# Performance work log

Hardware: AMD Instinct MI355X
Metric: run time of the kernel (lower is better)

Reference implementation:

```python
import jax, jax.numpy as jnp
import numpy as np

B, F, E, H, D = 8192, 40, 128, 4, 4
DH = E // H  # per-head attention dim
STD = 0.05   # all params init N(0, 0.05) in the torch module (including LayerNorm!)


def setup_inputs() -> dict:
    key = jax.random.key(0)
    ks = jax.random.split(key, 7)
    inputs = jax.random.normal(ks[0], (B, F, E), dtype=jnp.float32)
    # domain ids in [1, D] so every row belongs to some domain (torch masks domain_ids == i+1)
    domain_ids = jax.random.randint(ks[1], (B,), 1, D + 1)
    W_Queries = jax.random.normal(ks[2], (D, E, E), dtype=jnp.float32) * STD  # domain_W_Queries
    W_Value = jax.random.normal(ks[3], (E, E), dtype=jnp.float32) * STD
    W_Res = jax.random.normal(ks[4], (E, E), dtype=jnp.float32) * STD
    ln_gamma = jax.random.normal(ks[5], (D, E), dtype=jnp.float32) * STD  # per-domain LayerNorm weight
    ln_beta = jax.random.normal(ks[6], (D, E), dtype=jnp.float32) * STD   # per-domain LayerNorm bias
    return dict(inputs=inputs, domain_ids=domain_ids, W_Queries=W_Queries,
                W_Value=W_Value, W_Res=W_Res, ln_gamma=ln_gamma, ln_beta=ln_beta)


def reference(inputs, domain_ids, W_Queries, W_Value, W_Res, ln_gamma, ln_beta):
    d = domain_ids - 1  # (B,) zero-based domain index
    # value projection is shared across domains
    v = jnp.einsum('bfe,eh->bfh', inputs, W_Value).reshape(B, F, H, DH)
    # merge='no': the key projection is domain_W_Queries[0] for EVERY domain (source quirk)
    k = jnp.einsum('bfe,eh->bfh', inputs, W_Queries[0]).reshape(B, F, H, DH)
    # per-sample domain-routed query projection
    Wq_b = W_Queries[d]  # (B, E, E) gather
    q = jnp.einsum('bfe,beh->bfh', inputs, Wq_b).reshape(B, F, H, DH)
    # scaled multi-head attention over the field axis (F x F per head)
    scores = jnp.einsum('bihd,bjhd->bhij', q, k) / np.float32(np.sqrt(DH))
    attn = jax.nn.softmax(scores, axis=-1)  # attn_dropout is identity in eval mode
    out = jnp.einsum('bhij,bjhd->bihd', attn, v).reshape(B, F, E)
    # residual projection + relu
    out = jax.nn.relu(out + jnp.einsum('bfe,eh->bfh', inputs, W_Res))
    # per-domain LayerNorm (eps=1e-6), params gathered per sample
    mean = out.mean(axis=-1, keepdims=True)
    var = ((out - mean) ** 2).mean(axis=-1, keepdims=True)
    normed = (out - mean) / jnp.sqrt(var + 1e-6)
    return normed * ln_gamma[d][:, None, :] + ln_beta[d][:, None, :]
```

## Files before the change

kernel.cpp:

```cpp
#include <hip/hip_runtime.h>
#include <hip/hip_bf16.h>

typedef __attribute__((ext_vector_type(4))) float f32x4;
typedef __attribute__((ext_vector_type(8))) short s16x8;
typedef unsigned long long u64;

namespace {
constexpr int B_   = 8192;
constexpr int NT   = 256;
constexpr int SPB  = 8;
constexpr int NBLK = B_ / SPB;
constexpr int XS_SH  = 48 * 136;
constexpr int RED_B  = XS_SH * 2;
constexpr int OUT_B  = RED_B + 48 * 4 * 2 * 4;
constexpr int OSTR   = 132;
constexpr int POOL_B = OUT_B + 40 * OSTR * 4;
}

__device__ __forceinline__ ushort f2b(float f) {
    union { __hip_bfloat16 h; ushort u; } cv;
    cv.h = __float2bfloat16(f);
    return cv.u;
}
__device__ __forceinline__ u64 pack4(f32x4 v) {
    return (u64)f2b(v[0]) | ((u64)f2b(v[1]) << 16)
         | ((u64)f2b(v[2]) << 32) | ((u64)f2b(v[3]) << 48);
}
#define MFMA(a, b, c) __builtin_amdgcn_mfma_f32_16x16x32_bf16((a), (b), (c), 0, 0, 0)

__device__ __forceinline__ s16x8 remap(u64 A, u64 B, int sl0, int sl1, bool hi) {
    const int a0 = (int)A, a1 = (int)(A >> 32);
    const int b0 = (int)B, b1 = (int)(B >> 32);
    const int pa0 = __shfl(a0, sl0), pa2 = __shfl(a0, sl1);
    const int pa1 = __shfl(a1, sl0), pa3 = __shfl(a1, sl1);
    const int pb0 = __shfl(b0, sl0), pb2 = __shfl(b0, sl1);
    const int pb1 = __shfl(b1, sl0), pb3 = __shfl(b1, sl1);
    union { int i[4]; s16x8 v; } r;
    r.i[0] = hi ? pb0 : pa0;
    r.i[1] = hi ? pb1 : pa1;
    r.i[2] = hi ? pb2 : pa2;
    r.i[3] = hi ? pb3 : pa3;
    return r.v;
}
__device__ __forceinline__ s16x8 remapA(u64 A, int sl0, int sl1, bool hi) {
    const int a0 = (int)A, a1 = (int)(A >> 32);
    const int pa0 = __shfl(a0, sl0), pa2 = __shfl(a0, sl1);
    const int pa1 = __shfl(a1, sl0), pa3 = __shfl(a1, sl1);
    union { int i[4]; s16x8 v; } r;
    r.i[0] = hi ? 0 : pa0;
    r.i[1] = hi ? 0 : pa1;
    r.i[2] = hi ? 0 : pa2;
    r.i[3] = hi ? 0 : pa3;
    return r.v;
}

__global__ void convert_w(const float* __restrict__ Wq,
                          const float* __restrict__ Wv,
                          const float* __restrict__ Wr,
                          ushort* __restrict__ Wt)
{
    int idx = blockIdx.x * 256 + threadIdx.x;
    if (idx >= 6 * 16384) return;
    int m = idx >> 14, r = idx & 16383, n = r >> 7, k = r & 127;
    float v;
    if (m < 4)       v = Wq[(size_t)m * 16384 + k * 128 + n];
    else if (m == 4) v = Wv[k * 128 + n];
    else             v = Wr[k * 128 + n];
    Wt[idx] = f2b(v);
}

__global__ __launch_bounds__(NT, 2)
void mdr_fused7(const float* __restrict__ inputs,
                const int* __restrict__ dom,
                const ushort* __restrict__ Wt,
                const float* __restrict__ ln_g,
                const float* __restrict__ ln_b,
                float* __restrict__ out)
{
    __shared__ __align__(16) char pool[POOL_B];
    ushort* sp = reinterpret_cast<ushort*>(pool);
    float* red = reinterpret_cast<float*>(pool + RED_B);
    float* ost = reinterpret_cast<float*>(pool + OUT_B);

    const int t = threadIdx.x;
    const int w = t >> 6, l = t & 63;
    const int lr = l & 15, lc = l >> 4;
    const int sl0 = lr + 32 * (lc & 1);
    const int sl1 = sl0 + 16;
    const bool hi = lc >= 2;
    const int h = w;
    const size_t s0 = (size_t)blockIdx.x * SPB;
    const float4* in4 = reinterpret_cast<const float4*>(inputs);
    float4* out4g = reinterpret_cast<float4*>(out);

    {
        const int row = 40 + (t >> 5), c = (t & 31) * 4;
        *reinterpret_cast<u64*>(&sp[row * 136 + c]) = 0ull;
    }

    float4 xp[5];
    #pragma unroll
    for (int j = 0; j < 5; ++j)
        xp[j] = in4[s0 * 1280 + t + 256 * j];

    #pragma unroll 1
    for (int s = 0; s < SPB; ++s) {
        #pragma unroll
        for (int j = 0; j < 5; ++j) {
            const int idx4 = t + 256 * j;
            const int row = idx4 >> 5, c4 = idx4 & 31;
            u64 pk = (u64)f2b(xp[j].x) | ((u64)f2b(xp[j].y) << 16)
                   | ((u64)f2b(xp[j].z) << 32) | ((u64)f2b(xp[j].w) << 48);
            *reinterpret_cast<u64*>(&sp[row * 136 + c4 * 4]) = pk;
        }
        const int d = dom[s0 + s] - 1;
        __syncthreads();

        const ushort* wq = Wt + (size_t)d * 16384 + (h * 32) * 128;
        const ushort* wk = Wt + (h * 32) * 128;
        const ushort* wv = Wt + (size_t)4 * 16384 + (h * 32) * 128;
        const ushort* wr = Wt + (size_t)5 * 16384 + (h * 32) * 128;
        const int wo = lr * 128 + lc * 8;

        f32x4 aq[2][3], ak[2][3];
        #pragma unroll
        for (int nt = 0; nt < 2; ++nt)
            #pragma unroll
            for (int rt = 0; rt < 3; ++rt) {
                aq[nt][rt] = f32x4{0.f, 0.f, 0.f, 0.f};
                ak[nt][rt] = f32x4{0.f, 0.f, 0.f, 0.f};
            }
        #pragma unroll
        for (int kk = 0; kk < 4; ++kk) {
            s16x8 xf[3];
            #pragma unroll
            for (int rt = 0; rt < 3; ++rt)
                xf[rt] = *reinterpret_cast<const s16x8*>(&sp[(rt * 16 + lr) * 136 + kk * 32 + lc * 8]);
            #pragma unroll
            for (int nt = 0; nt < 2; ++nt) {
                const int o = nt * 2048 + wo + kk * 32;
                const s16x8 qf = *reinterpret_cast<const s16x8*>(wq + o);
                const s16x8 kf = *reinterpret_cast<const s16x8*>(wk + o);
                #pragma unroll
                for (int rt = 0; rt < 3; ++rt) {
                    aq[nt][rt] = MFMA(qf, xf[rt], aq[nt][rt]);
                    ak[nt][rt] = MFMA(kf, xf[rt], ak[nt][rt]);
                }
            }
        }
        s16x8 qfr[3], kfr[3];
        #pragma unroll
        for (int tt = 0; tt < 3; ++tt) {
            qfr[tt] = remap(pack4(aq[0][tt]), pack4(aq[1][tt]), sl0, sl1, hi);
            kfr[tt] = remap(pack4(ak[0][tt]), pack4(ak[1][tt]), sl0, sl1, hi);
        }

        f32x4 av[3][2], ar[2][3];
        #pragma unroll
        for (int nt = 0; nt < 2; ++nt)
            #pragma unroll
            for (int rt = 0; rt < 3; ++rt) {
                av[rt][nt] = f32x4{0.f, 0.f, 0.f, 0.f};
                ar[nt][rt] = f32x4{0.f, 0.f, 0.f, 0.f};
            }
        #pragma unroll
        for (int kk = 0; kk < 4; ++kk) {
            s16x8 xf[3];
            #pragma unroll
            for (int rt = 0; rt < 3; ++rt)
                xf[rt] = *reinterpret_cast<const s16x8*>(&sp[(rt * 16 + lr) * 136 + kk * 32 + lc * 8]);
            #pragma unroll
            for (int nt = 0; nt < 2; ++nt) {
                const int o = nt * 2048 + wo + kk * 32;
                const s16x8 vf = *reinterpret_cast<const s16x8*>(wv + o);
                const s16x8 rf = *reinterpret_cast<const s16x8*>(wr + o);
                #pragma unroll
                for (int rt = 0; rt < 3; ++rt) {
                    av[rt][nt] = MFMA(xf[rt], vf, av[rt][nt]);
                    ar[nt][rt] = MFMA(rf, xf[rt], ar[nt][rt]);
                }
            }
        }
        u64 pkV[3][2];
        #pragma unroll
        for (int rt = 0; rt < 3; ++rt)
            #pragma unroll
            for (int nt = 0; nt < 2; ++nt)
                pkV[rt][nt] = pack4(av[rt][nt]);

        const float scale = 0.17677669529663689f;
        u64 pkP[3][3];
        float inv[3];
        #pragma unroll
        for (int it = 0; it < 3; ++it) {
            f32x4 sr[3];
            #pragma unroll
            for (int jt = 0; jt < 3; ++jt) {
                f32x4 z = {0.f, 0.f, 0.f, 0.f};
                sr[jt] = MFMA(kfr[jt], qfr[it], z);
            }
            float sum = 0.f;
            #pragma unroll
            for (int jt = 0; jt < 3; ++jt) {
                f32x4 pv;
                #pragma unroll
                for (int reg = 0; reg < 4; ++reg) {
                    float p = (jt == 2 && lc >= 2) ? 0.f : __expf(sr[jt][reg] * scale);
                    pv[reg] = p;
                    sum += p;
                }
                pkP[it][jt] = pack4(pv);
            }
            sum += __shfl_xor(sum, 16);
            sum += __shfl_xor(sum, 32);
            inv[it] = 1.f / sum;
        }

        if (s + 1 < SPB) {
            #pragma unroll
            for (int j = 0; j < 5; ++j)
                xp[j] = in4[(s0 + s + 1) * 1280 + t + 256 * j];
        }

        f32x4 o[2][3];
        #pragma unroll
        for (int et = 0; et < 2; ++et)
            #pragma unroll
            for (int it = 0; it < 3; ++it)
                o[et][it] = f32x4{0.f, 0.f, 0.f, 0.f};
        #pragma unroll
        for (int kk = 0; kk < 2; ++kk) {
            s16x8 vfr[2], pfr[3];
            #pragma unroll
            for (int et = 0; et < 2; ++et)
                vfr[et] = kk ? remapA(pkV[2][et], sl0, sl1, hi)
                             : remap(pkV[0][et], pkV[1][et], sl0, sl1, hi);
            #pragma unroll
            for (int it = 0; it < 3; ++it)
                pfr[it] = kk ? remapA(pkP[it][2], sl0, sl1, hi)
                             : remap(pkP[it][0], pkP[it][1], sl0, sl1, hi);
            #pragma unroll
            for (int et = 0; et < 2; ++et)
                #pragma unroll
                for (int it = 0; it < 3; ++it)
                    o[et][it] = MFMA(vfr[et], pfr[it], o[et][it]);
        }

        #pragma unroll
        for (int it = 0; it < 3; ++it) {
            const bool valid = !(it == 2 && lr >= 8);
            float sa = 0.f, qa2 = 0.f;
            float4 yv[2];
            #pragma unroll
            for (int et = 0; et < 2; ++et)
                #pragma unroll
                for (int reg = 0; reg < 4; ++reg) {
                    float yy = fmaxf(fmaf(o[et][it][reg], inv[it], ar[et][it][reg]), 0.f);
                    (&yv[et].x)[reg] = yy;
                    sa += yy;
                    qa2 = fmaf(yy, yy, qa2);
                }
            sa  += __shfl_xor(sa, 16);   sa  += __shfl_xor(sa, 32);
            qa2 += __shfl_xor(qa2, 16);  qa2 += __shfl_xor(qa2, 32);
            if (lc == 0)
                *reinterpret_cast<float2*>(&red[((it * 16 + lr) * 4 + w) * 2]) =
                    make_float2(sa, qa2);
            if (valid) {
                #pragma unroll
                for (int et = 0; et < 2; ++et)
                    *reinterpret_cast<float4*>(&ost[(it * 16 + lr) * OSTR + h * 32 + et * 16 + 4 * lc]) = yv[et];
            }
        }
        __syncthreads();

        const int c4r = t & 31;
        const float4 gvr = *reinterpret_cast<const float4*>(&ln_g[d * 128 + c4r * 4]);
        const float4 bvr = *reinterpret_cast<const float4*>(&ln_b[d * 128 + c4r * 4]);
        const size_t b4 = (s0 + s) * 1280;
        #pragma unroll
        for (int j5 = 0; j5 < 5; ++j5) {
            const int idx = j5 * 256 + t;
            const int row = idx >> 5;
            const float4 r01 = *reinterpret_cast<const float4*>(&red[row * 8]);
            const float4 r23 = *reinterpret_cast<const float4*>(&red[row * 8 + 4]);
            const float sa = r01.x + r01.z + r23.x + r23.z;
            const float q2 = r01.y + r01.w + r23.y + r23.w;
            const float mean = sa * (1.f / 128.f);
            const float rstd = rsqrtf(q2 * (1.f / 128.f) - mean * mean + 1e-6f);
            const float4 v = *reinterpret_cast<const float4*>(&ost[row * OSTR + c4r * 4]);
            float4 ov;
            ov.x = (v.x - mean) * rstd * gvr.x + bvr.x;
            ov.y = (v.y - mean) * rstd * gvr.y + bvr.y;
            ov.z = (v.z - mean) * rstd * gvr.z + bvr.z;
            ov.w = (v.w - mean) * rstd * gvr.w + bvr.w;
            out4g[b4 + idx] = ov;
        }
    }
}

extern "C" void kernel_launch(void* const* d_in, const int* in_sizes, int n_in,
                              void* d_out, int out_size, void* d_ws, size_t ws_size,
                              hipStream_t stream)
{
    const float* inputs = (const float*)d_in[0];
    const int*   dm     = (const int*)d_in[1];
    const float* Wq     = (const float*)d_in[2];
    const float* Wv     = (const float*)d_in[3];
    const float* Wr     = (const float*)d_in[4];
    const float* g      = (const float*)d_in[5];
    const float* bt     = (const float*)d_in[6];
    float* outp         = (float*)d_out;
    ushort* Wt          = (ushort*)d_ws;

    convert_w<<<(6 * 16384 + 255) / 256, 256, 0, stream>>>(Wq, Wv, Wr, Wt);
    mdr_fused7<<<NBLK, NT, 0, stream>>>(inputs, dm, Wt, g, bt, outp);
}
```

Before: 152.9 us.

## Fuse Q/K/V/R projection loops, halve samples per block, use raw v_exp

Merges the two projection k-loops into one pass so each x fragment read from LDS feeds all four weight MFMAs. Accumulators are zero-initialized via the first MFMA instead of explicit zeroing. Samples per block drop from 8 to 4, doubling the grid to 2048 blocks. The softmax exp is computed with an inline v_exp_f32 using a log2-prescaled constant. The fused loop keeps 24 accumulators live at once, which raises register pressure under the occupancy-2 launch bound and risks spills.

```diff
diff --git a/kernel.cpp b/kernel.cpp
--- a/kernel.cpp
+++ b/kernel.cpp
@@ -8,7 +8,7 @@
 namespace {
 constexpr int B_   = 8192;
 constexpr int NT   = 256;
-constexpr int SPB  = 8;
+constexpr int SPB  = 4;
 constexpr int NBLK = B_ / SPB;
 constexpr int XS_SH  = 48 * 136;
 constexpr int RED_B  = XS_SH * 2;
@@ -70,7 +70,7 @@
 }
 
 __global__ __launch_bounds__(NT, 2)
-void mdr_fused7(const float* __restrict__ inputs,
+void mdr_fused8(const float* __restrict__ inputs,
                 const int* __restrict__ dom,
                 const ushort* __restrict__ Wt,
                 const float* __restrict__ ln_g,
@@ -122,14 +122,8 @@
         const ushort* wr = Wt + (size_t)5 * 16384 + (h * 32) * 128;
         const int wo = lr * 128 + lc * 8;
 
-        f32x4 aq[2][3], ak[2][3];
-        #pragma unroll
-        for (int nt = 0; nt < 2; ++nt)
-            #pragma unroll
-            for (int rt = 0; rt < 3; ++rt) {
-                aq[nt][rt] = f32x4{0.f, 0.f, 0.f, 0.f};
-                ak[nt][rt] = f32x4{0.f, 0.f, 0.f, 0.f};
-            }
+        f32x4 aq[2][3], ak[2][3], av[3][2], ar[2][3];
+        const f32x4 zz = {0.f, 0.f, 0.f, 0.f};
         #pragma unroll
         for (int kk = 0; kk < 4; ++kk) {
             s16x8 xf[3];
@@ -141,10 +135,14 @@
                 const int o = nt * 2048 + wo + kk * 32;
                 const s16x8 qf = *reinterpret_cast<const s16x8*>(wq + o);
                 const s16x8 kf = *reinterpret_cast<const s16x8*>(wk + o);
+                const s16x8 vf = *reinterpret_cast<const s16x8*>(wv + o);
+                const s16x8 rf = *reinterpret_cast<const s16x8*>(wr + o);
                 #pragma unroll
                 for (int rt = 0; rt < 3; ++rt) {
-                    aq[nt][rt] = MFMA(qf, xf[rt], aq[nt][rt]);
-                    ak[nt][rt] = MFMA(kf, xf[rt], ak[nt][rt]);
+                    aq[nt][rt] = MFMA(qf, xf[rt], kk == 0 ? zz : aq[nt][rt]);
+                    ak[nt][rt] = MFMA(kf, xf[rt], kk == 0 ? zz : ak[nt][rt]);
+                    av[rt][nt] = MFMA(xf[rt], vf, kk == 0 ? zz : av[rt][nt]);
+                    ar[nt][rt] = MFMA(rf, xf[rt], kk == 0 ? zz : ar[nt][rt]);
                 }
             }
         }
@@ -154,33 +152,6 @@
             qfr[tt] = remap(pack4(aq[0][tt]), pack4(aq[1][tt]), sl0, sl1, hi);
             kfr[tt] = remap(pack4(ak[0][tt]), pack4(ak[1][tt]), sl0, sl1, hi);
         }
-
-        f32x4 av[3][2], ar[2][3];
-        #pragma unroll
-        for (int nt = 0; nt < 2; ++nt)
-            #pragma unroll
-            for (int rt = 0; rt < 3; ++rt) {
-                av[rt][nt] = f32x4{0.f, 0.f, 0.f, 0.f};
-                ar[nt][rt] = f32x4{0.f, 0.f, 0.f, 0.f};
-            }
-        #pragma unroll
-        for (int kk = 0; kk < 4; ++kk) {
-            s16x8 xf[3];
-            #pragma unroll
-            for (int rt = 0; rt < 3; ++rt)
-                xf[rt] = *reinterpret_cast<const s16x8*>(&sp[(rt * 16 + lr) * 136 + kk * 32 + lc * 8]);
-            #pragma unroll
-            for (int nt = 0; nt < 2; ++nt) {
-                const int o = nt * 2048 + wo + kk * 32;
-                const s16x8 vf = *reinterpret_cast<const s16x8*>(wv + o);
-                const s16x8 rf = *reinterpret_cast<const s16x8*>(wr + o);
-                #pragma unroll
-                for (int rt = 0; rt < 3; ++rt) {
-                    av[rt][nt] = MFMA(xf[rt], vf, av[rt][nt]);
-                    ar[nt][rt] = MFMA(rf, xf[rt], ar[nt][rt]);
-                }
-            }
-        }
         u64 pkV[3][2];
         #pragma unroll
         for (int rt = 0; rt < 3; ++rt)
@@ -188,7 +159,7 @@
             for (int nt = 0; nt < 2; ++nt)
                 pkV[rt][nt] = pack4(av[rt][nt]);
 
-        const float scale = 0.17677669529663689f;
+        const float l2scale = 0.2550348615f;
         u64 pkP[3][3];
         float inv[3];
         #pragma unroll
@@ -205,7 +176,13 @@
                 f32x4 pv;
                 #pragma unroll
                 for (int reg = 0; reg < 4; ++reg) {
-                    float p = (jt == 2 && lc >= 2) ? 0.f : __expf(sr[jt][reg] * scale);
+                    float p;
+                    if (jt == 2 && lc >= 2) {
+                        p = 0.f;
+                    } else {
+                        const float e2 = sr[jt][reg] * l2scale;
+                        asm("v_exp_f32 %0, %1" : "=v"(p) : "v"(e2));
+                    }
                     pv[reg] = p;
                     sum += p;
                 }
@@ -313,5 +290,5 @@
     ushort* Wt          = (ushort*)d_ws;
 
     convert_w<<<(6 * 16384 + 255) / 256, 256, 0, stream>>>(Wq, Wv, Wr, Wt);
-    mdr_fused7<<<NBLK, NT, 0, stream>>>(inputs, dm, Wt, g, bt, outp);
-}
+    mdr_fused8<<<NBLK, NT, 0, stream>>>(inputs, dm, Wt, g, bt, outp);
+}
```

After: 231.7 us. +51.5%, slower.
